# Kernel tuning notes

Hardware: AMD Instinct MI355X
Metric: run time of the kernel (lower is better)

## Reference

```python
import jax, jax.numpy as jnp
import numpy as np

IN_SIZE = 4096
OUT_SIZE = 4096
NUM_ROWS = 256
NUM_COLS = 256
IN_BLOCKS = 16   # ceil(4096/256)
OUT_BLOCKS = 16
BATCH = 128
QUANTIZE = 'log'
QUANTIZE_BITS = 8
G_INF = 2.0
G_MIN = 0.001
TAU = 0.75


def rram_quantize(w, tau, g_inf, g_min, bits, mode):
    """Snap each element of w to the nearest of 2**bits RRAM conductance levels.
    mode='log': saturating-exponential pulse model; mode='linear': uniform levels.
    Vectorized over the whole array (equivalent to the original per-element vmap).
    """
    L = 2 ** bits
    n = jnp.arange(L, dtype=w.dtype)
    if mode == 'log':
        scale = (g_inf - g_min) / (1.0 - jnp.exp(jnp.asarray(-tau, w.dtype)))
        levels = g_min + scale * (1.0 - jnp.exp(-tau * n / (L - 1)))
    else:
        levels = g_min + (g_inf - g_min) * n / (L - 1)
    # levels is monotonically increasing -> nearest-level via searchsorted
    idx = jnp.clip(jnp.searchsorted(levels, w), 1, L - 1)
    lo = levels[idx - 1]
    hi = levels[idx]
    return jnp.where(w - lo < hi - w, lo, hi)


def setup_inputs() -> dict:
    key = jax.random.key(0)
    kx, kc = jax.random.split(key)
    x = jax.random.normal(kx, (BATCH, IN_SIZE), dtype=jnp.float32)
    # glorot_normal over last two dims (fan_in=num_cols, fan_out=num_rows)
    std = float(np.sqrt(2.0 / (NUM_ROWS + NUM_COLS)))
    cores = std * jax.random.normal(kc, (OUT_BLOCKS, IN_BLOCKS, NUM_ROWS, NUM_COLS), dtype=jnp.float32)
    return {'x': x, 'cores': cores}


def reference(x, cores):
    # pad input to in_blocks * num_rows and split into blocks
    pad = NUM_ROWS * IN_BLOCKS - IN_SIZE  # = 0 here, kept for faithfulness
    x_padded = jnp.pad(x, ((0, 0), (0, pad)))
    x_blocks = x_padded.reshape(x.shape[0], IN_BLOCKS, NUM_ROWS)  # (b, j, l)
    # relu then RRAM quantization of the cores
    w = jax.nn.relu(cores)
    w = rram_quantize(w, TAU, G_INF, G_MIN, QUANTIZE_BITS, QUANTIZE)
    # blockwise batched matmul: (i,j,k,l),(b,j,l)->(b,i,j,k)
    y = jnp.einsum('ijkl,bjl->bijk', w, x_blocks)
    return y
```

## Files before the change

### kernel.cpp

```cpp
#include <hip/hip_runtime.h>
#include <hip/hip_bf16.h>
#include <math.h>


typedef __attribute__((ext_vector_type(4))) float f32x4;
typedef __attribute__((ext_vector_type(8))) short bf16x8;
typedef __attribute__((ext_vector_type(4))) short s16x4;

#define TAU   0.75f
#define G_INF 2.0f
#define G_MIN 0.001f

__device__ __forceinline__ short f2bf_rne(float f) {
    union { float f; unsigned u; } v; v.f = f;
    unsigned u = v.u;
    return (short)((u + 0x7FFFu + ((u >> 16) & 1u)) >> 16);
}

__global__ __launch_bounds__(256, 4)
void bd_fused(const float* __restrict__ x,
              const float* __restrict__ cores,
              float* __restrict__ out)
{
    __shared__ float levels[256];
    __shared__ unsigned char wq[64 * 512];

    const int tid = threadIdx.x;

    {
        float n = (float)tid;
        float a = -TAU * n;
        a = a / 255.0f;
        float e = expf(a);
        float scale = (G_INF - G_MIN) / (1.0f - expf(-TAU));
        levels[tid] = G_MIN + scale * (1.0f - e);
    }
    __syncthreads();

    const int bid = blockIdx.x;
    const int ns = bid & 3;
    const int j  = (bid >> 2) & 15;
    const int i  = bid >> 6;

    const float scale     = (G_INF - G_MIN) / (1.0f - expf(-TAU));
    const float inv_scale = 1.0f / scale;
    const float kn = -(255.0f / TAU) * 0.69314718055994531f;

    const float* wsrc = cores + (((size_t)(i * 16 + j)) << 16) + ((size_t)ns << 14);
    #pragma unroll
    for (int it = 0; it < 16; ++it) {
        int e = it * 1024 + tid * 4;
        f32x4 v = *(const f32x4*)(wsrc + e);
        s16x4 q;
        #pragma unroll
        for (int c = 0; c < 4; ++c) {
            float w = fmaxf(v[c], 0.0f);
            float t = 1.0f - (w - G_MIN) * inv_scale;
            t = fmaxf(t, 1e-20f);
            float nr = kn * __log2f(t);
            int f = (int)floorf(nr);
            f = f < 0 ? 0 : (f > 254 ? 254 : f);
            float lo = levels[f];
            float hi = levels[f + 1];
            float qv = (w - lo < hi - w) ? lo : hi;
            q[c] = f2bf_rne(qv);
        }
        int r  = e >> 8;
        int kb = (e & 255) * 2;
        int off = (r * 512 + kb) ^ ((r & 7) << 4);
        *(s16x4*)(wq + off) = q;
    }
    __syncthreads();

    const int wave  = tid >> 6;
    const int lane  = tid & 63;
    const int l15   = lane & 15;
    const int l4    = lane >> 4;
    const int brow0 = wave * 32;

    f32x4 acc[2][4];
    #pragma unroll
    for (int mt = 0; mt < 2; ++mt)
        #pragma unroll
        for (int nt = 0; nt < 4; ++nt)
            acc[mt][nt] = (f32x4){0.f, 0.f, 0.f, 0.f};

    const float* xb0 = x + (size_t)(brow0 + l15) * 4096 + j * 256 + l4 * 8;

    #pragma unroll
    for (int s = 0; s < 8; ++s) {
        bf16x8 afr[2];
        #pragma unroll
        for (int mt = 0; mt < 2; ++mt) {
            const float* xp = xb0 + mt * (16 * 4096) + s * 32;
            f32x4 v0 = *(const f32x4*)xp;
            f32x4 v1 = *(const f32x4*)(xp + 4);
            bf16x8 a;
            a[0] = f2bf_rne(v0[0]); a[1] = f2bf_rne(v0[1]);
            a[2] = f2bf_rne(v0[2]); a[3] = f2bf_rne(v0[3]);
            a[4] = f2bf_rne(v1[0]); a[5] = f2bf_rne(v1[1]);
            a[6] = f2bf_rne(v1[2]); a[7] = f2bf_rne(v1[3]);
            afr[mt] = a;
        }
        #pragma unroll
        for (int nt = 0; nt < 4; ++nt) {
            int r   = nt * 16 + l15;
            int off = (r * 512 + s * 64 + l4 * 16) ^ ((r & 7) << 4);
            bf16x8 bfr = *(const bf16x8*)(wq + off);
            acc[0][nt] = __builtin_amdgcn_mfma_f32_16x16x32_bf16(afr[0], bfr, acc[0][nt], 0, 0, 0);
            acc[1][nt] = __builtin_amdgcn_mfma_f32_16x16x32_bf16(afr[1], bfr, acc[1][nt], 0, 0, 0);
        }
    }

    #pragma unroll
    for (int mt = 0; mt < 2; ++mt) {
        #pragma unroll
        for (int nt = 0; nt < 4; ++nt) {
            int k = (ns << 6) + nt * 16 + l15;
            #pragma unroll
            for (int v = 0; v < 4; ++v) {
                int b = brow0 + mt * 16 + l4 * 4 + v;
                out[((size_t)((b * 16 + i) * 16 + j) << 8) + k] = acc[mt][nt][v];
            }
        }
    }
}

extern "C" void kernel_launch(void* const* d_in, const int* in_sizes, int n_in,
                              void* d_out, int out_size, void* d_ws, size_t ws_size,
                              hipStream_t stream) {
    const float* x     = (const float*)d_in[0];
    const float* cores = (const float*)d_in[1];
    float* out = (float*)d_out;
    bd_fused<<<dim3(1024), dim3(256), 0, stream>>>(x, cores, out);
}
```

Before: 31.68 us.

## Swap MFMA operands for vectorized output stores, prefetch weights, pair LUT levels

Swaps the MFMA A/B operands so each lane's accumulator holds four consecutive k outputs. This lets the epilogue write one 16-byte vector store per tile instead of four scalar strided stores. All 16 weight vector loads are now issued before the barrier so they overlap the LUT setup, and the level table stores lo/hi pairs so one shared-memory read fetches both neighbours. Holding 16 prefetched vectors raises register pressure under the 4-blocks-per-SM launch bound.

```diff
diff --git a/kernel.cpp b/kernel.cpp
--- a/kernel.cpp
+++ b/kernel.cpp
@@ -4,6 +4,7 @@
 
 
 typedef __attribute__((ext_vector_type(4))) float f32x4;
+typedef __attribute__((ext_vector_type(2))) float f32x2;
 typedef __attribute__((ext_vector_type(8))) short bf16x8;
 typedef __attribute__((ext_vector_type(4))) short s16x4;
 
@@ -17,25 +18,29 @@
     return (short)((u + 0x7FFFu + ((u >> 16) & 1u)) >> 16);
 }
 
+__device__ __forceinline__ float level_of(float n) {
+    float a = (-TAU) * n;
+    a = a / 255.0f;
+    float e = expf(a);
+    float scale = (G_INF - G_MIN) / (1.0f - expf(-TAU));
+    return G_MIN + scale * (1.0f - e);
+}
+
 __global__ __launch_bounds__(256, 4)
 void bd_fused(const float* __restrict__ x,
               const float* __restrict__ cores,
               float* __restrict__ out)
 {
-    __shared__ float levels[256];
+    __shared__ f32x2 lut2[256];
     __shared__ unsigned char wq[64 * 512];
 
     const int tid = threadIdx.x;
 
     {
-        float n = (float)tid;
-        float a = -TAU * n;
-        a = a / 255.0f;
-        float e = expf(a);
-        float scale = (G_INF - G_MIN) / (1.0f - expf(-TAU));
-        levels[tid] = G_MIN + scale * (1.0f - e);
+        float lo = level_of((float)tid);
+        float hi = level_of((float)(tid < 255 ? tid + 1 : 255));
+        lut2[tid] = (f32x2){lo, hi};
     }
-    __syncthreads();
 
     const int bid = blockIdx.x;
     const int ns = bid & 3;
@@ -47,10 +52,16 @@
     const float kn = -(255.0f / TAU) * 0.69314718055994531f;
 
     const float* wsrc = cores + (((size_t)(i * 16 + j)) << 16) + ((size_t)ns << 14);
+    f32x4 wv[16];
+    #pragma unroll
+    for (int it = 0; it < 16; ++it)
+        wv[it] = *(const f32x4*)(wsrc + it * 1024 + tid * 4);
+
+    __syncthreads();
+
     #pragma unroll
     for (int it = 0; it < 16; ++it) {
-        int e = it * 1024 + tid * 4;
-        f32x4 v = *(const f32x4*)(wsrc + e);
+        f32x4 v = wv[it];
         s16x4 q;
         #pragma unroll
         for (int c = 0; c < 4; ++c) {
@@ -60,11 +71,11 @@
             float nr = kn * __log2f(t);
             int f = (int)floorf(nr);
             f = f < 0 ? 0 : (f > 254 ? 254 : f);
-            float lo = levels[f];
-            float hi = levels[f + 1];
-            float qv = (w - lo < hi - w) ? lo : hi;
+            f32x2 lh = lut2[f];
+            float qv = (w - lh.x < lh.y - w) ? lh.x : lh.y;
             q[c] = f2bf_rne(qv);
         }
+        int e  = it * 1024 + tid * 4;
         int r  = e >> 8;
         int kb = (e & 255) * 2;
         int off = (r * 512 + kb) ^ ((r & 7) << 4);
@@ -78,50 +89,47 @@
     const int l4    = lane >> 4;
     const int brow0 = wave * 32;
 
-    f32x4 acc[2][4];
+    f32x4 acc[4][2];
     #pragma unroll
-    for (int mt = 0; mt < 2; ++mt)
+    for (int nt = 0; nt < 4; ++nt)
         #pragma unroll
-        for (int nt = 0; nt < 4; ++nt)
-            acc[mt][nt] = (f32x4){0.f, 0.f, 0.f, 0.f};
+        for (int mt = 0; mt < 2; ++mt)
+            acc[nt][mt] = (f32x4){0.f, 0.f, 0.f, 0.f};
 
     const float* xb0 = x + (size_t)(brow0 + l15) * 4096 + j * 256 + l4 * 8;
 
     #pragma unroll
     for (int s = 0; s < 8; ++s) {
-        bf16x8 afr[2];
+        bf16x8 bfr[2];
         #pragma unroll
         for (int mt = 0; mt < 2; ++mt) {
             const float* xp = xb0 + mt * (16 * 4096) + s * 32;
             f32x4 v0 = *(const f32x4*)xp;
             f32x4 v1 = *(const f32x4*)(xp + 4);
-            bf16x8 a;
-            a[0] = f2bf_rne(v0[0]); a[1] = f2bf_rne(v0[1]);
-            a[2] = f2bf_rne(v0[2]); a[3] = f2bf_rne(v0[3]);
-            a[4] = f2bf_rne(v1[0]); a[5] = f2bf_rne(v1[1]);
-            a[6] = f2bf_rne(v1[2]); a[7] = f2bf_rne(v1[3]);
-            afr[mt] = a;
+            bf16x8 b;
+            b[0] = f2bf_rne(v0[0]); b[1] = f2bf_rne(v0[1]);
+            b[2] = f2bf_rne(v0[2]); b[3] = f2bf_rne(v0[3]);
+            b[4] = f2bf_rne(v1[0]); b[5] = f2bf_rne(v1[1]);
+            b[6] = f2bf_rne(v1[2]); b[7] = f2bf_rne(v1[3]);
+            bfr[mt] = b;
         }
         #pragma unroll
         for (int nt = 0; nt < 4; ++nt) {
             int r   = nt * 16 + l15;
             int off = (r * 512 + s * 64 + l4 * 16) ^ ((r & 7) << 4);
-            bf16x8 bfr = *(const bf16x8*)(wq + off);
-            acc[0][nt] = __builtin_amdgcn_mfma_f32_16x16x32_bf16(afr[0], bfr, acc[0][nt], 0, 0, 0);
-            acc[1][nt] = __builtin_amdgcn_mfma_f32_16x16x32_bf16(afr[1], bfr, acc[1][nt], 0, 0, 0);
+            bf16x8 afr = *(const bf16x8*)(wq + off);
+            acc[nt][0] = __builtin_amdgcn_mfma_f32_16x16x32_bf16(afr, bfr[0], acc[nt][0], 0, 0, 0);
+            acc[nt][1] = __builtin_amdgcn_mfma_f32_16x16x32_bf16(afr, bfr[1], acc[nt][1], 0, 0, 0);
         }
     }
 
     #pragma unroll
-    for (int mt = 0; mt < 2; ++mt) {
+    for (int nt = 0; nt < 4; ++nt) {
         #pragma unroll
-        for (int nt = 0; nt < 4; ++nt) {
-            int k = (ns << 6) + nt * 16 + l15;
-            #pragma unroll
-            for (int v = 0; v < 4; ++v) {
-                int b = brow0 + mt * 16 + l4 * 4 + v;
-                out[((size_t)((b * 16 + i) * 16 + j) << 8) + k] = acc[mt][nt][v];
-            }
+        for (int mt = 0; mt < 2; ++mt) {
+            int b  = brow0 + mt * 16 + l15;
+            int kg = (ns << 6) + nt * 16 + (l4 << 2);
+            *(f32x4*)(out + (((size_t)((b * 16 + i) * 16 + j)) << 8) + kg) = acc[nt][mt];
         }
     }
 }
```

New measurement: 31.96 us. No clear change (+0.9%).

## Quantize weights straight into MFMA registers, pre-convert x to bf16, vectorize stores

Applied to the files above, without the earlier changes.

Each wave now loads its own 16 weight rows and quantizes them directly into MFMA A-fragments held in registers. This removes the shared-memory staging, the level table and both block barriers, and rebuilds each quantization level with exp2 instead of a table lookup. The MMA operands are swapped so every wave covers all 128 batch rows for its 16 output columns, which lets the output be written as contiguous float4 stores. A separate pre-pass converts x to bf16 in workspace so x loads are halved, at the cost of an extra kernel launch and more register pressure.

```diff
diff --git a/kernel.cpp b/kernel.cpp
--- a/kernel.cpp
+++ b/kernel.cpp
@@ -5,7 +5,7 @@
 
 typedef __attribute__((ext_vector_type(4))) float f32x4;
 typedef __attribute__((ext_vector_type(8))) short bf16x8;
-typedef __attribute__((ext_vector_type(4))) short s16x4;
+typedef __attribute__((ext_vector_type(8))) short s16x8;
 
 #define TAU   0.75f
 #define G_INF 2.0f
@@ -17,112 +17,110 @@
     return (short)((u + 0x7FFFu + ((u >> 16) & 1u)) >> 16);
 }
 
+__global__ __launch_bounds__(256)
+void xcvt(const float* __restrict__ xin, short* __restrict__ xbf) {
+    int idx = (blockIdx.x * 256 + threadIdx.x) * 8;
+    f32x4 a = *(const f32x4*)(xin + idx);
+    f32x4 b = *(const f32x4*)(xin + idx + 4);
+    s16x8 o;
+    o[0] = f2bf_rne(a[0]); o[1] = f2bf_rne(a[1]);
+    o[2] = f2bf_rne(a[2]); o[3] = f2bf_rne(a[3]);
+    o[4] = f2bf_rne(b[0]); o[5] = f2bf_rne(b[1]);
+    o[6] = f2bf_rne(b[2]); o[7] = f2bf_rne(b[3]);
+    *(s16x8*)(xbf + idx) = o;
+}
+
+template<bool XBF>
 __global__ __launch_bounds__(256, 4)
 void bd_fused(const float* __restrict__ x,
+              const short* __restrict__ xbf,
               const float* __restrict__ cores,
               float* __restrict__ out)
 {
-    __shared__ float levels[256];
-    __shared__ unsigned char wq[64 * 512];
-
-    const int tid = threadIdx.x;
-
-    {
-        float n = (float)tid;
-        float a = -TAU * n;
-        a = a / 255.0f;
-        float e = expf(a);
-        float scale = (G_INF - G_MIN) / (1.0f - expf(-TAU));
-        levels[tid] = G_MIN + scale * (1.0f - e);
-    }
-    __syncthreads();
+    const int tid  = threadIdx.x;
+    const int wave = tid >> 6;
+    const int lane = tid & 63;
+    const int l15  = lane & 15;
+    const int l4   = lane >> 4;
 
     const int bid = blockIdx.x;
-    const int ns = bid & 3;
-    const int j  = (bid >> 2) & 15;
-    const int i  = bid >> 6;
+    const int ns  = bid & 3;
+    const int j   = (bid >> 2) & 15;
+    const int i   = bid >> 6;
+    const int k0  = ns * 64 + wave * 16;
 
     const float scale     = (G_INF - G_MIN) / (1.0f - expf(-TAU));
     const float inv_scale = 1.0f / scale;
     const float kn = -(255.0f / TAU) * 0.69314718055994531f;
+    const float c2 = -(TAU / 255.0f) * 1.44269504088896341f;
+    const float Ac = G_MIN + scale;
+    const float Bc = scale * (1.0f - expf(-TAU / 255.0f));
 
-    const float* wsrc = cores + (((size_t)(i * 16 + j)) << 16) + ((size_t)ns << 14);
+    const float* wrow = cores + (((size_t)(i * 16 + j)) << 16)
+                              + (size_t)(k0 + l15) * 256 + l4 * 8;
+    bf16x8 afr[8];
     #pragma unroll
-    for (int it = 0; it < 16; ++it) {
-        int e = it * 1024 + tid * 4;
-        f32x4 v = *(const f32x4*)(wsrc + e);
-        s16x4 q;
+    for (int h = 0; h < 2; ++h) {
+        f32x4 wv[4][2];
         #pragma unroll
-        for (int c = 0; c < 4; ++c) {
-            float w = fmaxf(v[c], 0.0f);
-            float t = 1.0f - (w - G_MIN) * inv_scale;
-            t = fmaxf(t, 1e-20f);
-            float nr = kn * __log2f(t);
-            int f = (int)floorf(nr);
-            f = f < 0 ? 0 : (f > 254 ? 254 : f);
-            float lo = levels[f];
-            float hi = levels[f + 1];
-            float qv = (w - lo < hi - w) ? lo : hi;
-            q[c] = f2bf_rne(qv);
+        for (int s4 = 0; s4 < 4; ++s4) {
+            const float* p = wrow + (h * 4 + s4) * 32;
+            wv[s4][0] = *(const f32x4*)p;
+            wv[s4][1] = *(const f32x4*)(p + 4);
         }
-        int r  = e >> 8;
-        int kb = (e & 255) * 2;
-        int off = (r * 512 + kb) ^ ((r & 7) << 4);
-        *(s16x4*)(wq + off) = q;
+        #pragma unroll
+        for (int s4 = 0; s4 < 4; ++s4) {
+            bf16x8 a;
+            #pragma unroll
+            for (int e = 0; e < 8; ++e) {
+                float w = fmaxf(wv[s4][e >> 2][e & 3], 0.0f);
+                float t = 1.0f - (w - G_MIN) * inv_scale;
+                t = fmaxf(t, 1e-8f);
+                float nr = kn * __log2f(t);
+                int f = (int)floorf(nr);
+                f = f < 0 ? 0 : (f > 254 ? 254 : f);
+                float ef = exp2f(c2 * (float)f);
+                float lo = Ac - scale * ef;
+                float hi = lo + Bc * ef;
+                float qv = (w - lo < hi - w) ? lo : hi;
+                a[e] = f2bf_rne(qv);
+            }
+            afr[h * 4 + s4] = a;
+        }
     }
-    __syncthreads();
 
-    const int wave  = tid >> 6;
-    const int lane  = tid & 63;
-    const int l15   = lane & 15;
-    const int l4    = lane >> 4;
-    const int brow0 = wave * 32;
+    f32x4 acc[8];
+    #pragma unroll
+    for (int mt = 0; mt < 8; ++mt) acc[mt] = (f32x4){0.f, 0.f, 0.f, 0.f};
 
-    f32x4 acc[2][4];
-    #pragma unroll
-    for (int mt = 0; mt < 2; ++mt)
-        #pragma unroll
-        for (int nt = 0; nt < 4; ++nt)
-            acc[mt][nt] = (f32x4){0.f, 0.f, 0.f, 0.f};
-
-    const float* xb0 = x + (size_t)(brow0 + l15) * 4096 + j * 256 + l4 * 8;
+    const short* xb = xbf + (size_t)l15 * 4096 + j * 256 + l4 * 8;
+    const float* xf = x   + (size_t)l15 * 4096 + j * 256 + l4 * 8;
 
     #pragma unroll
     for (int s = 0; s < 8; ++s) {
-        bf16x8 afr[2];
         #pragma unroll
-        for (int mt = 0; mt < 2; ++mt) {
-            const float* xp = xb0 + mt * (16 * 4096) + s * 32;
-            f32x4 v0 = *(const f32x4*)xp;
-            f32x4 v1 = *(const f32x4*)(xp + 4);
-            bf16x8 a;
-            a[0] = f2bf_rne(v0[0]); a[1] = f2bf_rne(v0[1]);
-            a[2] = f2bf_rne(v0[2]); a[3] = f2bf_rne(v0[3]);
-            a[4] = f2bf_rne(v1[0]); a[5] = f2bf_rne(v1[1]);
-            a[6] = f2bf_rne(v1[2]); a[7] = f2bf_rne(v1[3]);
-            afr[mt] = a;
-        }
-        #pragma unroll
-        for (int nt = 0; nt < 4; ++nt) {
-            int r   = nt * 16 + l15;
-            int off = (r * 512 + s * 64 + l4 * 16) ^ ((r & 7) << 4);
-            bf16x8 bfr = *(const bf16x8*)(wq + off);
-            acc[0][nt] = __builtin_amdgcn_mfma_f32_16x16x32_bf16(afr[0], bfr, acc[0][nt], 0, 0, 0);
-            acc[1][nt] = __builtin_amdgcn_mfma_f32_16x16x32_bf16(afr[1], bfr, acc[1][nt], 0, 0, 0);
+        for (int mt = 0; mt < 8; ++mt) {
+            bf16x8 bfr;
+            if (XBF) {
+                bfr = *(const bf16x8*)(xb + (size_t)mt * 65536 + s * 32);
+            } else {
+                const float* p = xf + (size_t)mt * 65536 + s * 32;
+                f32x4 v0 = *(const f32x4*)p;
+                f32x4 v1 = *(const f32x4*)(p + 4);
+                bfr[0] = f2bf_rne(v0[0]); bfr[1] = f2bf_rne(v0[1]);
+                bfr[2] = f2bf_rne(v0[2]); bfr[3] = f2bf_rne(v0[3]);
+                bfr[4] = f2bf_rne(v1[0]); bfr[5] = f2bf_rne(v1[1]);
+                bfr[6] = f2bf_rne(v1[2]); bfr[7] = f2bf_rne(v1[3]);
+            }
+            acc[mt] = __builtin_amdgcn_mfma_f32_16x16x32_bf16(afr[s], bfr, acc[mt], 0, 0, 0);
         }
     }
 
     #pragma unroll
-    for (int mt = 0; mt < 2; ++mt) {
-        #pragma unroll
-        for (int nt = 0; nt < 4; ++nt) {
-            int k = (ns << 6) + nt * 16 + l15;
-            #pragma unroll
-            for (int v = 0; v < 4; ++v) {
-                int b = brow0 + mt * 16 + l4 * 4 + v;
-                out[((size_t)((b * 16 + i) * 16 + j) << 8) + k] = acc[mt][nt][v];
-            }
-        }
+    for (int mt = 0; mt < 8; ++mt) {
+        int b = mt * 16 + l15;
+        size_t o = (((size_t)((b * 16 + i) * 16 + j)) << 8) + k0 + (l4 << 2);
+        *(f32x4*)(out + o) = acc[mt];
     }
 }
 
@@ -132,5 +130,13 @@
     const float* x     = (const float*)d_in[0];
     const float* cores = (const float*)d_in[1];
     float* out = (float*)d_out;
-    bd_fused<<<dim3(1024), dim3(256), 0, stream>>>(x, cores, out);
+
+    const size_t xbytes = (size_t)128 * 4096 * sizeof(short);
+    if (ws_size >= xbytes) {
+        short* xbf = (short*)d_ws;
+        xcvt<<<dim3(256), dim3(256), 0, stream>>>(x, xbf);
+        bd_fused<true><<<dim3(1024), dim3(256), 0, stream>>>(x, xbf, cores, out);
+    } else {
+        bd_fused<false><<<dim3(1024), dim3(256), 0, stream>>>(x, nullptr, cores, out);
+    }
 }
```

Result: slower. 51.52 us (+62.6%).
